# Performance work log

Measured on AMD Instinct MI355X. Metric: run time of the kernel, lower is better.

Reference implementation:

```python
import jax, jax.numpy as jnp
import numpy as np

D_IN = 1024
D_OUT = 1024
N_HEADS = 16
HEAD_DIM = D_OUT // N_HEADS


def setup_inputs() -> dict:
    key = jax.random.key(0)
    ks = jax.random.split(key, 6)
    s = 0.02
    return {
        "x": jax.random.normal(ks[0], (2, 2048, D_IN), dtype=jnp.float32),
        "W_q": jax.random.normal(ks[1], (D_IN, D_OUT), dtype=jnp.float32) * s,
        "W_k": jax.random.normal(ks[2], (D_IN, D_OUT), dtype=jnp.float32) * s,
        "W_v": jax.random.normal(ks[3], (D_IN, D_OUT), dtype=jnp.float32) * s,
        "W_o": jax.random.normal(ks[4], (D_OUT, D_OUT), dtype=jnp.float32) * s,
        "b_o": jax.random.normal(ks[5], (D_OUT,), dtype=jnp.float32) * s,
    }


def reference(x, W_q, W_k, W_v, W_o, b_o):
    b, n, _ = x.shape
    # project and split heads: [b, h, n, d]
    q = (x @ W_q).reshape(b, n, N_HEADS, HEAD_DIM).transpose(0, 2, 1, 3)
    k = (x @ W_k).reshape(b, n, N_HEADS, HEAD_DIM).transpose(0, 2, 1, 3)
    v = (x @ W_v).reshape(b, n, N_HEADS, HEAD_DIM).transpose(0, 2, 1, 3)
    scores = jnp.einsum("bhqd,bhkd->bhqk", q, k)
    # causal mask: positions k > q masked with -inf (applied BEFORE scaling, as in source)
    causal = jnp.tril(jnp.ones((n, n), dtype=bool))
    scores = jnp.where(causal, scores, -jnp.inf)
    scale = HEAD_DIM ** 0.5
    attn = jax.nn.softmax(scores / scale, axis=-1)
    ctx = jnp.einsum("bhqk,bhkd->bhqd", attn, v)
    ctx = ctx.transpose(0, 2, 1, 3).reshape(b, n, D_OUT)
    return ctx @ W_o + b_o
```

## Files before the change

### kernel.cpp

```cpp
#include <hip/hip_runtime.h>
#include <hip/hip_bf16.h>


typedef __bf16 bf16x8 __attribute__((ext_vector_type(8)));
typedef __bf16 bf16x4 __attribute__((ext_vector_type(4)));
typedef float  f32x4  __attribute__((ext_vector_type(4)));

typedef __attribute__((address_space(1))) void gas_void;
typedef __attribute__((address_space(3))) void las_void;

__device__ __forceinline__ void gload_lds16(const void* g, void* l) {
  __builtin_amdgcn_global_load_lds((gas_void*)g, (las_void*)l, 16, 0, 0);
}

#define FULL_DRAIN() asm volatile("s_waitcnt vmcnt(0) lgkmcnt(0)" ::: "memory")
#define SCHED_FENCE() __builtin_amdgcn_sched_barrier(0)

#define QSCALE 0.18033688011112042f

__global__ void cvt_f32_bf16_k(const float* __restrict__ in, __bf16* __restrict__ out, int n4) {
  int i = blockIdx.x * 256 + threadIdx.x;
  if (i >= n4) return;
  float4 v = ((const float4*)in)[i];
  bf16x4 o = { (__bf16)v.x, (__bf16)v.y, (__bf16)v.z, (__bf16)v.w };
  ((bf16x4*)out)[i] = o;
}

__global__ void transpose_w4_k(const float* __restrict__ Wq, const float* __restrict__ Wk,
                               const float* __restrict__ Wv, const float* __restrict__ Wo,
                               __bf16* __restrict__ wtqkv, __bf16* __restrict__ wot) {
  __shared__ float tile[32][33];
  const int z = blockIdx.z;
  const float* in = z == 0 ? Wq : z == 1 ? Wk : z == 2 ? Wv : Wo;
  __bf16* out = z < 3 ? wtqkv + (size_t)z * 1048576 : wot;
  const int bx = blockIdx.x, by = blockIdx.y;
  const int tx = threadIdx.x, ty = threadIdx.y;
#pragma unroll
  for (int i = 0; i < 4; ++i)
    tile[ty + i * 8][tx] = in[(by * 32 + ty + i * 8) * 1024 + bx * 32 + tx];
  __syncthreads();
#pragma unroll
  for (int i = 0; i < 4; ++i)
    out[(size_t)(bx * 32 + ty + i * 8) * 1024 + by * 32 + tx] = (__bf16)tile[tx][ty + i * 8];
}

__device__ __forceinline__ bf16x8 lds_swz32(const __bf16* base, int row, int cb) {
  const char* p = (const char*)base + row * 64 + (cb ^ (((row >> 1) & 3) << 4));
  return *(const bf16x8*)p;
}

__global__ __launch_bounds__(256) void gemm_qkv_k(
    const __bf16* __restrict__ A, const __bf16* __restrict__ Bt,
    __bf16* __restrict__ qo, __bf16* __restrict__ ko, __bf16* __restrict__ vo)
{
  __shared__ __align__(16) __bf16 As[3][4096];
  __shared__ __align__(16) __bf16 Bs[3][4096];

  const int bm = blockIdx.x, bn = blockIdx.y;

  const int t = threadIdx.x;
  const int l = t & 63;
  const int w = t >> 6;
  const int wr = w >> 1, wc = w & 1;
  const int lr = l & 15;
  const int lkb = (l >> 4) * 16;

  const int swz_el = ((t & 3) * 8) ^ (((t >> 3) & 3) << 3);
  const __bf16* a0 = A + (size_t)(bm * 128 + (t >> 2)) * 1024 + swz_el;
  const __bf16* b0 = Bt + (size_t)(bn * 128 + (t >> 2)) * 1024 + swz_el;

  f32x4 acc[4][4] = {};

#define STAGE(kt_, buf_)                                          \
  do {                                                            \
    const int k0_ = (kt_) * 32;                                   \
    gload_lds16(a0 + k0_, As[buf_] + t * 8);                      \
    gload_lds16(a0 + 64 * 1024 + k0_, As[buf_] + 2048 + t * 8);   \
    gload_lds16(b0 + k0_, Bs[buf_] + t * 8);                      \
    gload_lds16(b0 + 64 * 1024 + k0_, Bs[buf_] + 2048 + t * 8);   \
  } while (0)

  STAGE(0, 0);
  STAGE(1, 1);
  SCHED_FENCE();
  asm volatile("s_waitcnt vmcnt(4)" ::: "memory");
  __builtin_amdgcn_s_barrier();
  SCHED_FENCE();

  int bc = 0, bs = 2;
  for (int kt = 0; kt < 32; ++kt) {
    if (kt < 30) STAGE(kt + 2, bs);
    SCHED_FENCE();

    bf16x8 af[4], bfr[4];
#pragma unroll
    for (int m = 0; m < 4; ++m)
      af[m] = lds_swz32(As[bc], wr * 64 + m * 16 + lr, lkb);
#pragma unroll
    for (int n = 0; n < 4; ++n)
      bfr[n] = lds_swz32(Bs[bc], wc * 64 + n * 16 + lr, lkb);
#pragma unroll
    for (int m = 0; m < 4; ++m)
#pragma unroll
      for (int n = 0; n < 4; ++n)
        acc[m][n] = __builtin_amdgcn_mfma_f32_16x16x32_bf16(af[m], bfr[n], acc[m][n], 0, 0, 0);

    SCHED_FENCE();
    if (kt < 30) asm volatile("s_waitcnt vmcnt(4)" ::: "memory");
    else         asm volatile("s_waitcnt vmcnt(0)" ::: "memory");
    __builtin_amdgcn_s_barrier();
    SCHED_FENCE();
    bc = (bc == 2) ? 0 : bc + 1;
    bs = (bs == 2) ? 0 : bs + 1;
  }
#undef STAGE

#pragma unroll
  for (int m = 0; m < 4; ++m) {
    const int rg = bm * 128 + wr * 64 + m * 16 + (l >> 4) * 4;
#pragma unroll
    for (int n = 0; n < 4; ++n) {
      const int cg = bn * 128 + wc * 64 + n * 16 + lr;
      const int proj = cg >> 10, within = cg & 1023;
      const int h = within >> 6, d = within & 63;
#pragma unroll
      for (int r = 0; r < 4; ++r) {
        const int row = rg + r;
        const int b = row >> 11, pos = row & 2047;
        const int bh = b * 16 + h;
        const float v = acc[m][n][r];
        if (proj == 0) {
          qo[((size_t)bh * 2048 + pos) * 64 + d] = (__bf16)(v * QSCALE);
        } else if (proj == 1) {
          const int tile = pos >> 6, rr = pos & 63;
          const int off = rr * 128 + ((d * 2) ^ ((rr & 7) << 4));
          *(__bf16*)((char*)ko + ((size_t)bh * 32 + tile) * 8192 + off) = (__bf16)v;
        } else {
          const int tile = pos >> 6, cc = pos & 63;
          const int off = d * 128 + ((cc * 2) ^ ((d & 7) << 4));
          *(__bf16*)((char*)vo + ((size_t)bh * 32 + tile) * 8192 + off) = (__bf16)v;
        }
      }
    }
  }
}

__global__ __launch_bounds__(256) void gemm_out_k(
    const __bf16* __restrict__ A, const __bf16* __restrict__ Bt,
    float* __restrict__ outf, const float* __restrict__ bias)
{
  __shared__ __align__(16) __bf16 As[3][4096];
  __shared__ __align__(16) __bf16 Bs[3][2048];

  const int bid = blockIdx.x;
  const int bm = bid & 31, bn = bid >> 5;

  const int t = threadIdx.x;
  const int l = t & 63;
  const int w = t >> 6;
  const int wr = w >> 1, wc = w & 1;
  const int lr = l & 15;
  const int lkb = (l >> 4) * 16;

  const int swz_el = ((t & 3) * 8) ^ (((t >> 3) & 3) << 3);
  const __bf16* a0 = A + (size_t)(bm * 128 + (t >> 2)) * 1024 + swz_el;
  const __bf16* b0 = Bt + (size_t)(bn * 64 + (t >> 2)) * 1024 + swz_el;

  f32x4 acc[4][2] = {};

#define STAGE(kt_, buf_)                                          \
  do {                                                            \
    const int k0_ = (kt_) * 32;                                   \
    gload_lds16(a0 + k0_, As[buf_] + t * 8);                      \
    gload_lds16(a0 + 64 * 1024 + k0_, As[buf_] + 2048 + t * 8);   \
    gload_lds16(b0 + k0_, Bs[buf_] + t * 8);                      \
  } while (0)

  STAGE(0, 0);
  STAGE(1, 1);
  SCHED_FENCE();
  asm volatile("s_waitcnt vmcnt(3)" ::: "memory");
  __builtin_amdgcn_s_barrier();
  SCHED_FENCE();

  int bc = 0, bs = 2;
  for (int kt = 0; kt < 32; ++kt) {
    if (kt < 30) STAGE(kt + 2, bs);
    SCHED_FENCE();

    bf16x8 af[4], bfr[2];
#pragma unroll
    for (int m = 0; m < 4; ++m)
      af[m] = lds_swz32(As[bc], wr * 64 + m * 16 + lr, lkb);
#pragma unroll
    for (int n = 0; n < 2; ++n)
      bfr[n] = lds_swz32(Bs[bc], wc * 32 + n * 16 + lr, lkb);
#pragma unroll
    for (int m = 0; m < 4; ++m)
#pragma unroll
      for (int n = 0; n < 2; ++n)
        acc[m][n] = __builtin_amdgcn_mfma_f32_16x16x32_bf16(af[m], bfr[n], acc[m][n], 0, 0, 0);

    SCHED_FENCE();
    if (kt < 30) asm volatile("s_waitcnt vmcnt(3)" ::: "memory");
    else         asm volatile("s_waitcnt vmcnt(0)" ::: "memory");
    __builtin_amdgcn_s_barrier();
    SCHED_FENCE();
    bc = (bc == 2) ? 0 : bc + 1;
    bs = (bs == 2) ? 0 : bs + 1;
  }
#undef STAGE

#pragma unroll
  for (int m = 0; m < 4; ++m) {
    const int rg = bm * 128 + wr * 64 + m * 16 + (l >> 4) * 4;
#pragma unroll
    for (int n = 0; n < 2; ++n) {
      const int cg = bn * 64 + wc * 32 + n * 16 + lr;
#pragma unroll
      for (int r = 0; r < 4; ++r)
        outf[(size_t)(rg + r) * 1024 + cg] = acc[m][n][r] + bias[cg];
    }
  }
}

__device__ __forceinline__ bf16x8 lds_swz(const __bf16* base, int row, int cb) {
  const char* p = (const char*)base + row * 128 + (cb ^ ((row & 7) << 4));
  return *(const bf16x8*)p;
}

__global__ __launch_bounds__(512) void attn_fwd_k(
    const __bf16* __restrict__ Q, const __bf16* __restrict__ K,
    const __bf16* __restrict__ V, __bf16* __restrict__ ctx)
{
  __shared__ __align__(16) char smem[53760];
  __bf16* Kbuf = (__bf16*)smem;
  __bf16* Vbuf = (__bf16*)(smem + 16384);
  __bf16* PsB  = (__bf16*)(smem + 32768);
  float*  LsX  = (float*)(smem + 53248);
  float*  xch  = (float*)smem;

  const int n = blockIdx.x;
  const int bh = (n & 255) >> 3;
  const int pp = n & 7;
  const int qt = (n >> 8) ? pp : 15 - pp;
  const int nkt = 2 * qt + 2;

  const int t = threadIdx.x, l = t & 63, w = t >> 6;
  const int lr = l & 15, lg = l >> 4;
  const int qb = w & 3;
  const int kvh = w >> 2;

  const __bf16* qptr = Q + (size_t)bh * 131072;
  const __bf16* kptr = K + (size_t)bh * 131072;
  const __bf16* vptr = V + (size_t)bh * 131072;
  __bf16* Ps = PsB + w * 1280;

  bf16x8 qf[2][2];
#pragma unroll
  for (int m = 0; m < 2; ++m)
#pragma unroll
    for (int h2 = 0; h2 < 2; ++h2)
      qf[m][h2] = *(const bf16x8*)(qptr + (size_t)(qt * 128 + qb * 32 + m * 16 + lr) * 64 + h2 * 32 + lg * 8);

  f32x4 o[2][4] = {};
  f32x4 lsum[2] = {};

  gload_lds16(kptr + t * 8, Kbuf + t * 8);
  gload_lds16(vptr + t * 8, Vbuf + t * 8);
  FULL_DRAIN();
  __syncthreads();
  SCHED_FENCE();

  for (int kt = 0; kt < nkt; ++kt) {
    const int cur = kt & 1;
    if (kt + 1 < nkt) {
      gload_lds16(kptr + (kt + 1) * 4096 + t * 8, Kbuf + (cur ^ 1) * 4096 + t * 8);
      gload_lds16(vptr + (kt + 1) * 4096 + t * 8, Vbuf + (cur ^ 1) * 4096 + t * 8);
    }
    SCHED_FENCE();
    const __bf16* Kb = Kbuf + cur * 4096;
    const __bf16* Vb = Vbuf + cur * 4096;

    bf16x8 kf[2][2];
#pragma unroll
    for (int ng = 0; ng < 2; ++ng)
#pragma unroll
      for (int h2 = 0; h2 < 2; ++h2)
        kf[ng][h2] = lds_swz(Kb, kvh * 32 + ng * 16 + lr, h2 * 64 + lg * 16);

    f32x4 s[2][2];
#pragma unroll
    for (int m = 0; m < 2; ++m)
#pragma unroll
      for (int ng = 0; ng < 2; ++ng) {
        f32x4 z = {};
        z = __builtin_amdgcn_mfma_f32_16x16x32_bf16(qf[m][0], kf[ng][0], z, 0, 0, 0);
        s[m][ng] = __builtin_amdgcn_mfma_f32_16x16x32_bf16(qf[m][1], kf[ng][1], z, 0, 0, 0);
      }

    if (kt >= 2 * qt) {
#pragma unroll
      for (int m = 0; m < 2; ++m) {
        const int qpos = qt * 128 + qb * 32 + m * 16 + lg * 4;
#pragma unroll
        for (int ng = 0; ng < 2; ++ng) {
          const int kv = kt * 64 + kvh * 32 + ng * 16 + lr;
#pragma unroll
          for (int r = 0; r < 4; ++r)
            if (kv > qpos + r) s[m][ng][r] = -1e30f;
        }
      }
    }

#pragma unroll
    for (int m = 0; m < 2; ++m)
#pragma unroll
      for (int ng = 0; ng < 2; ++ng)
#pragma unroll
        for (int r = 0; r < 4; ++r) {
          const float p = __builtin_amdgcn_exp2f(s[m][ng][r]);
          lsum[m][r] += p;
          Ps[(m * 16 + lg * 4 + r) * 40 + ng * 16 + lr] = (__bf16)p;
        }

    asm volatile("s_waitcnt lgkmcnt(0)" ::: "memory");
    SCHED_FENCE();

    bf16x8 pf[2];
#pragma unroll
    for (int m = 0; m < 2; ++m)
      pf[m] = *(const bf16x8*)(Ps + (m * 16 + lr) * 40 + lg * 8);
    bf16x8 vf[4];
#pragma unroll
    for (int ngd = 0; ngd < 4; ++ngd)
      vf[ngd] = lds_swz(Vb, ngd * 16 + lr, kvh * 64 + lg * 16);
#pragma unroll
    for (int m = 0; m < 2; ++m)
#pragma unroll
      for (int ngd = 0; ngd < 4; ++ngd)
        o[m][ngd] = __builtin_amdgcn_mfma_f32_16x16x32_bf16(pf[m], vf[ngd], o[m][ngd], 0, 0, 0);

    FULL_DRAIN();
    __syncthreads();
    SCHED_FENCE();
  }

#pragma unroll
  for (int m = 0; m < 2; ++m)
#pragma unroll
    for (int r = 0; r < 4; ++r) {
      float v = lsum[m][r];
      v += __shfl_xor(v, 1);
      v += __shfl_xor(v, 2);
      v += __shfl_xor(v, 4);
      v += __shfl_xor(v, 8);
      lsum[m][r] = v;
    }

  if (kvh == 1) {
#pragma unroll
    for (int m = 0; m < 2; ++m)
#pragma unroll
      for (int ngd = 0; ngd < 4; ++ngd)
#pragma unroll
        for (int r = 0; r < 4; ++r)
          xch[qb * 2048 + (m * 16 + lg * 4 + r) * 64 + ngd * 16 + lr] = o[m][ngd][r];
    if (lr == 0) {
#pragma unroll
      for (int m = 0; m < 2; ++m)
#pragma unroll
        for (int r = 0; r < 4; ++r)
          LsX[qb * 32 + m * 16 + lg * 4 + r] = lsum[m][r];
    }
  }
  FULL_DRAIN();
  __syncthreads();
  SCHED_FENCE();

  if (kvh == 0) {
    const int b_ = bh >> 4, h = bh & 15;
#pragma unroll
    for (int m = 0; m < 2; ++m)
#pragma unroll
      for (int r = 0; r < 4; ++r) {
        const float sum = lsum[m][r] + LsX[qb * 32 + m * 16 + lg * 4 + r];
        const float inv = 1.0f / sum;
        const int pos = qt * 128 + qb * 32 + m * 16 + lg * 4 + r;
#pragma unroll
        for (int ngd = 0; ngd < 4; ++ngd) {
          const float val = o[m][ngd][r] +
              xch[qb * 2048 + (m * 16 + lg * 4 + r) * 64 + ngd * 16 + lr];
          ctx[((size_t)(b_ * 2048 + pos)) * 1024 + h * 64 + ngd * 16 + lr] =
              (__bf16)(val * inv);
        }
      }
  }
}

extern "C" void kernel_launch(void* const* d_in, const int* in_sizes, int n_in,
                              void* d_out, int out_size, void* d_ws, size_t ws_size,
                              hipStream_t stream) {
  const float* x  = (const float*)d_in[0];
  const float* Wq = (const float*)d_in[1];
  const float* Wk = (const float*)d_in[2];
  const float* Wv = (const float*)d_in[3];
  const float* Wo = (const float*)d_in[4];
  const float* bo = (const float*)d_in[5];
  float* out = (float*)d_out;

  char* ws = (char*)d_ws;
  __bf16* xb    = (__bf16*)(ws);
  __bf16* wtqkv = (__bf16*)(ws + (8u << 20));
  __bf16* wot   = (__bf16*)(ws + (14u << 20));
  __bf16* qbuf  = (__bf16*)(ws + (16u << 20));
  __bf16* kbuf  = (__bf16*)(ws + (24u << 20));
  __bf16* vbuf  = (__bf16*)(ws + (32u << 20));
  __bf16* ctx   = (__bf16*)(ws + (40u << 20));

  cvt_f32_bf16_k<<<4096, 256, 0, stream>>>(x, xb, 1048576);
  transpose_w4_k<<<dim3(32, 32, 4), dim3(32, 8), 0, stream>>>(Wq, Wk, Wv, Wo, wtqkv, wot);

  gemm_qkv_k<<<dim3(32, 24), 256, 0, stream>>>(xb, wtqkv, qbuf, kbuf, vbuf);
  attn_fwd_k<<<512, 512, 0, stream>>>(qbuf, kbuf, vbuf, ctx);
  gemm_out_k<<<512, 256, 0, stream>>>(ctx, wot, out, bo);
}
```

Baseline: 103.6 us.

## Triple-buffer K/V tiles in attention kernel with partial vmcnt waits

Attention K/V staging moves from double to triple buffering. Loads are issued two tiles ahead, and each iteration ends with a partial vmcnt wait instead of a full drain, so the next tile's global-to-LDS load can stay in flight across the barrier. V fragment LDS reads are also hoisted to just after the K reads, ahead of the softmax. LDS use grows to about 70KB per block, which may reduce occupancy, and the ordering relies on per-thread vmcnt before the raw s_barrier.

Result: slower. 108.4 us (+4.7%).

```diff
diff --git a/kernel.cpp b/kernel.cpp
--- a/kernel.cpp
+++ b/kernel.cpp
@@ -233,11 +233,11 @@
     const __bf16* __restrict__ Q, const __bf16* __restrict__ K,
     const __bf16* __restrict__ V, __bf16* __restrict__ ctx)
 {
-  __shared__ __align__(16) char smem[53760];
+  __shared__ __align__(16) char smem[70144];
   __bf16* Kbuf = (__bf16*)smem;
-  __bf16* Vbuf = (__bf16*)(smem + 16384);
-  __bf16* PsB  = (__bf16*)(smem + 32768);
-  float*  LsX  = (float*)(smem + 53248);
+  __bf16* Vbuf = (__bf16*)(smem + 24576);
+  __bf16* PsB  = (__bf16*)(smem + 49152);
+  float*  LsX  = (float*)(smem + 69632);
   float*  xch  = (float*)smem;
 
   const int n = blockIdx.x;
@@ -266,21 +266,25 @@
   f32x4 o[2][4] = {};
   f32x4 lsum[2] = {};
 
-  gload_lds16(kptr + t * 8, Kbuf + t * 8);
-  gload_lds16(vptr + t * 8, Vbuf + t * 8);
-  FULL_DRAIN();
-  __syncthreads();
-  SCHED_FENCE();
-
+#define ASTAGE(kt_, buf_)                                                  \
+  do {                                                                     \
+    gload_lds16(kptr + (kt_) * 4096 + t * 8, Kbuf + (buf_) * 4096 + t * 8); \
+    gload_lds16(vptr + (kt_) * 4096 + t * 8, Vbuf + (buf_) * 4096 + t * 8); \
+  } while (0)
+
+  ASTAGE(0, 0);
+  ASTAGE(1, 1);
+  SCHED_FENCE();
+  asm volatile("s_waitcnt vmcnt(2)" ::: "memory");
+  __builtin_amdgcn_s_barrier();
+  SCHED_FENCE();
+
+  int bc = 0, bs = 2;
   for (int kt = 0; kt < nkt; ++kt) {
-    const int cur = kt & 1;
-    if (kt + 1 < nkt) {
-      gload_lds16(kptr + (kt + 1) * 4096 + t * 8, Kbuf + (cur ^ 1) * 4096 + t * 8);
-      gload_lds16(vptr + (kt + 1) * 4096 + t * 8, Vbuf + (cur ^ 1) * 4096 + t * 8);
-    }
-    SCHED_FENCE();
-    const __bf16* Kb = Kbuf + cur * 4096;
-    const __bf16* Vb = Vbuf + cur * 4096;
+    if (kt + 2 < nkt) ASTAGE(kt + 2, bs);
+    SCHED_FENCE();
+    const __bf16* Kb = Kbuf + bc * 4096;
+    const __bf16* Vb = Vbuf + bc * 4096;
 
     bf16x8 kf[2][2];
 #pragma unroll
@@ -288,6 +292,10 @@
 #pragma unroll
       for (int h2 = 0; h2 < 2; ++h2)
         kf[ng][h2] = lds_swz(Kb, kvh * 32 + ng * 16 + lr, h2 * 64 + lg * 16);
+    bf16x8 vf[4];
+#pragma unroll
+    for (int ngd = 0; ngd < 4; ++ngd)
+      vf[ngd] = lds_swz(Vb, ngd * 16 + lr, kvh * 64 + lg * 16);
 
     f32x4 s[2][2];
 #pragma unroll
@@ -331,20 +339,21 @@
 #pragma unroll
     for (int m = 0; m < 2; ++m)
       pf[m] = *(const bf16x8*)(Ps + (m * 16 + lr) * 40 + lg * 8);
-    bf16x8 vf[4];
-#pragma unroll
-    for (int ngd = 0; ngd < 4; ++ngd)
-      vf[ngd] = lds_swz(Vb, ngd * 16 + lr, kvh * 64 + lg * 16);
 #pragma unroll
     for (int m = 0; m < 2; ++m)
 #pragma unroll
       for (int ngd = 0; ngd < 4; ++ngd)
         o[m][ngd] = __builtin_amdgcn_mfma_f32_16x16x32_bf16(pf[m], vf[ngd], o[m][ngd], 0, 0, 0);
 
-    FULL_DRAIN();
-    __syncthreads();
-    SCHED_FENCE();
-  }
+    SCHED_FENCE();
+    if (kt + 2 < nkt) asm volatile("s_waitcnt vmcnt(2)" ::: "memory");
+    else              asm volatile("s_waitcnt vmcnt(0)" ::: "memory");
+    __builtin_amdgcn_s_barrier();
+    SCHED_FENCE();
+    bc = (bc == 2) ? 0 : bc + 1;
+    bs = (bs == 2) ? 0 : bs + 1;
+  }
+#undef ASTAGE
 
 #pragma unroll
   for (int m = 0; m < 2; ++m)
```
